# Optimization experiments

Measured on AMD Instinct MI355X. Metric: run time of the kernel, lower is better.

## Reference

```python
import jax, jax.numpy as jnp
import numpy as np

F = 20  # hard-coded feature width in the module


def setup_inputs() -> dict:
    key = jax.random.key(0)
    k1, k2, k3, k4 = jax.random.split(key, 4)
    N = 1048576
    x = jax.random.normal(k1, (N, F), dtype=jnp.float32)
    # nn.Linear(20, 20): weight [out, in], bias [out]
    W = jax.random.normal(k2, (F, F), dtype=jnp.float32) * (1.0 / np.sqrt(F))
    b = jax.random.normal(k3, (F,), dtype=jnp.float32) * 0.01
    rand_weight = jax.random.normal(k4, (F, F), dtype=jnp.float32)
    return {"x": x, "W": W, "b": b, "rand_weight": rand_weight}


def _halving_count(s):
    """Smallest int k >= 0 with s * 2^-k <= 1 (== number of `x /= 2` loop iters)."""
    k = jnp.ceil(jnp.log2(jnp.maximum(s, 1.0))).astype(jnp.int32)
    # guard against float rounding in log2
    k = jnp.where(s * jnp.exp2(-k.astype(jnp.float32)) > 1.0, k + 1, k)
    k = jnp.where((k > 0) & (s * jnp.exp2(-(k - 1).astype(jnp.float32)) <= 1.0), k - 1, k)
    return k


def reference(x, W, b, rand_weight):
    # x = self.linear(x)
    h = x @ W.T + b
    # x = relu(x @ rand_weight + 1)
    h = jax.nn.relu(h @ rand_weight + 1.0)
    # x = self.linear(x)  (shared weights)
    h = h @ W.T + b
    # while x.abs().sum() > 1: x /= 2   ->  x * 2^-k
    s = jnp.sum(jnp.abs(h))
    k = _halving_count(s)
    h = h * jnp.exp2(-k.astype(h.dtype))
    return jnp.sum(h)
```

## Files before the change

kernel.cpp:

```cpp
#include <hip/hip_runtime.h>
#include <math.h>

#define FF 20
#define TPB 256
#define TPW 8

typedef __fp16 half2v __attribute__((ext_vector_type(2)));
typedef __fp16 half8 __attribute__((ext_vector_type(8)));
typedef float f32x4 __attribute__((ext_vector_type(4)));

__global__ void mlp_setup(const float* __restrict__ W, const float* __restrict__ b,
                          const float* __restrict__ R, __fp16* __restrict__ frag) {
    int t = threadIdx.x;
    int f = t >> 6, l = t & 63;
    int g = l >> 4, p = l & 15;
    int row = (f & 1) * 16 + p;
    #pragma unroll
    for (int e = 0; e < 8; ++e) {
        int k = (e < 4) ? (4 * g + e) : (16 + 4 * g + (e - 4));
        float v = 0.f;
        if (f < 2) {
            if (row < FF) {
                if (k < FF) {
                    float s = 0.f;
                    for (int j = 0; j < FF; ++j) s = fmaf(W[j * FF + k], R[j * FF + row], s);
                    v = s;
                } else if (k == FF) {
                    float s = 1.0f;
                    for (int j = 0; j < FF; ++j) s = fmaf(b[j], R[j * FF + row], s);
                    v = s;
                }
            }
        } else {
            if (row < FF) {
                if (k < FF) v = W[row * FF + k];
                else if (k == FF) v = b[row];
            }
        }
        frag[t * 8 + e] = (__fp16)v;
    }
}

__global__ __launch_bounds__(TPB) void mlp_main(
    const float* __restrict__ x, const __fp16* __restrict__ frag,
    double2* __restrict__ partials, int nrows, int ntiles)
{
    const int t = threadIdx.x;
    const int l = t & 63;
    const int g = l >> 4;
    const int r = l & 15;

    const half8 A10 = *reinterpret_cast<const half8*>(frag + (0 * 64 + l) * 8);
    const half8 A11 = *reinterpret_cast<const half8*>(frag + (1 * 64 + l) * 8);
    const half8 A20 = *reinterpret_cast<const half8*>(frag + (2 * 64 + l) * 8);
    const half8 A21 = *reinterpret_cast<const half8*>(frag + (3 * 64 + l) * 8);

    const int wave_id = blockIdx.x * (TPB / 64) + (t >> 6);
    const int base_row = wave_id * (TPW * 16) + r;

    float4 xa[TPW], xb[TPW];
    const float* rowp = x + (size_t)base_row * FF;
    #pragma unroll
    for (int u = 0; u < TPW; ++u) {
        int row = base_row + u * 16;
        xa[u] = make_float4(0.f, 0.f, 0.f, 0.f);
        if (row < nrows)
            xa[u] = *reinterpret_cast<const float4*>(rowp + (size_t)u * 16 * FF + 4 * g);
    }
    #pragma unroll
    for (int u = 0; u < TPW; ++u) {
        int row = base_row + u * 16;
        xb[u] = make_float4(0.f, 0.f, 0.f, 0.f);
        if (g == 0 && row < nrows)
            xb[u] = *reinterpret_cast<const float4*>(rowp + (size_t)u * 16 * FF + 16);
    }

    float psum = 0.f, pabs = 0.f;
    const f32x4 zero = {0.f, 0.f, 0.f, 0.f};

    #pragma unroll
    for (int u = 0; u < TPW; ++u) {
        half8 B1;
        half2v p0 = __builtin_amdgcn_cvt_pkrtz(xa[u].x, xa[u].y);
        half2v p1 = __builtin_amdgcn_cvt_pkrtz(xa[u].z, xa[u].w);
        B1[0] = p0[0]; B1[1] = p0[1]; B1[2] = p1[0]; B1[3] = p1[1];
        if (g == 0) {
            half2v p2 = __builtin_amdgcn_cvt_pkrtz(xb[u].x, xb[u].y);
            half2v p3 = __builtin_amdgcn_cvt_pkrtz(xb[u].z, xb[u].w);
            B1[4] = p2[0]; B1[5] = p2[1]; B1[6] = p3[0]; B1[7] = p3[1];
        } else if (g == 1) {
            B1[4] = (__fp16)1.0f;
            B1[5] = (__fp16)0.f; B1[6] = (__fp16)0.f; B1[7] = (__fp16)0.f;
        } else {
            B1[4] = (__fp16)0.f; B1[5] = (__fp16)0.f;
            B1[6] = (__fp16)0.f; B1[7] = (__fp16)0.f;
        }
        f32x4 c0 = __builtin_amdgcn_mfma_f32_16x16x32_f16(A10, B1, zero, 0, 0, 0);
        f32x4 c1 = __builtin_amdgcn_mfma_f32_16x16x32_f16(A11, B1, zero, 0, 0, 0);
        half8 B2;
        half2v q0 = __builtin_amdgcn_cvt_pkrtz(fmaxf(c0[0], 0.f), fmaxf(c0[1], 0.f));
        half2v q1 = __builtin_amdgcn_cvt_pkrtz(fmaxf(c0[2], 0.f), fmaxf(c0[3], 0.f));
        half2v q2 = __builtin_amdgcn_cvt_pkrtz(fmaxf(c1[0], 0.f), fmaxf(c1[1], 0.f));
        half2v q3 = __builtin_amdgcn_cvt_pkrtz(fmaxf(c1[2], 0.f), fmaxf(c1[3], 0.f));
        B2[0] = q0[0]; B2[1] = q0[1]; B2[2] = q1[0]; B2[3] = q1[1];
        B2[4] = q2[0]; B2[5] = q2[1]; B2[6] = q3[0]; B2[7] = q3[1];
        if (g == 1) B2[4] = (__fp16)1.0f;
        f32x4 d0 = __builtin_amdgcn_mfma_f32_16x16x32_f16(A20, B2, zero, 0, 0, 0);
        f32x4 d1 = __builtin_amdgcn_mfma_f32_16x16x32_f16(A21, B2, zero, 0, 0, 0);
        if (base_row + u * 16 < nrows) {
            #pragma unroll
            for (int q = 0; q < 4; ++q) {
                psum += d0[q];            pabs += fabsf(d0[q]);
                psum += d1[q];            pabs += fabsf(d1[q]);
            }
        }
    }

    #pragma unroll
    for (int off = 32; off > 0; off >>= 1) {
        psum += __shfl_down(psum, off, 64);
        pabs += __shfl_down(pabs, off, 64);
    }
    __shared__ double wsum[TPB / 64], wabs[TPB / 64];
    if ((t & 63) == 0) { wsum[t >> 6] = (double)psum; wabs[t >> 6] = (double)pabs; }
    __syncthreads();
    if (t == 0) {
        double bs = 0.0, ba = 0.0;
        #pragma unroll
        for (int w = 0; w < TPB / 64; ++w) { bs += wsum[w]; ba += wabs[w]; }
        partials[blockIdx.x] = make_double2(bs, ba);
    }
}

__global__ __launch_bounds__(256) void mlp_final(const double2* __restrict__ parts,
                                                 int nparts, float* __restrict__ out) {
    __shared__ double s_sum[256], s_abs[256];
    int t = threadIdx.x;
    double a = 0.0, sg = 0.0;
    for (int i = t; i < nparts; i += 256) { sg += parts[i].x; a += parts[i].y; }
    s_sum[t] = sg; s_abs[t] = a;
    __syncthreads();
    for (int off = 128; off > 0; off >>= 1) {
        if (t < off) { s_sum[t] += s_sum[t + off]; s_abs[t] += s_abs[t + off]; }
        __syncthreads();
    }
    if (t == 0) {
        double s = s_abs[0];
        int k = 0;
        while (s > 1.0 && k < 4000) { s *= 0.5; ++k; }
        out[0] = (float)ldexp(s_sum[0], -k);
    }
}

extern "C" void kernel_launch(void* const* d_in, const int* in_sizes, int n_in,
                              void* d_out, int out_size, void* d_ws, size_t ws_size,
                              hipStream_t stream) {
    const float* x = (const float*)d_in[0];
    const float* W = (const float*)d_in[1];
    const float* b = (const float*)d_in[2];
    const float* R = (const float*)d_in[3];
    float* out = (float*)d_out;

    __fp16* frag = (__fp16*)d_ws;
    double2* partials = (double2*)((char*)d_ws + 8192);

    int nrows = in_sizes[0] / FF;
    int ntiles = (nrows + 15) / 16;
    int waves = (ntiles + TPW - 1) / TPW;
    int blocks = (waves + (TPB / 64) - 1) / (TPB / 64);

    hipLaunchKernelGGL(mlp_setup, dim3(1), dim3(256), 0, stream, W, b, R, frag);
    hipLaunchKernelGGL(mlp_main, dim3(blocks), dim3(TPB), 0, stream,
                       x, frag, partials, nrows, ntiles);
    hipLaunchKernelGGL(mlp_final, dim3(1), dim3(256), 0, stream, partials, blocks, out);
}
```

Baseline: 30.76 us.

## Fuse weight-fragment setup into main kernel via per-wave MFMA precompute

Removes the separate single-block setup kernel and instead has every wave build its MFMA A-fragments directly from W, b and R, computing W^T·R (plus the bias row) with four small MFMAs in registers. This drops one kernel launch and its serialization ahead of the main kernel, at the cost of redundant scattered global loads of the weights and extra MFMAs in every wave. It also splits the load and compute path into a full-tile branch with no per-row bounds checks and a guarded tail branch. Precision changes slightly because the fused matrix is now formed from fp16-rounded inputs instead of being computed in fp32.

```diff
diff --git a/kernel.cpp b/kernel.cpp
--- a/kernel.cpp
+++ b/kernel.cpp
@@ -9,111 +9,130 @@
 typedef __fp16 half8 __attribute__((ext_vector_type(8)));
 typedef float f32x4 __attribute__((ext_vector_type(4)));
 
-__global__ void mlp_setup(const float* __restrict__ W, const float* __restrict__ b,
-                          const float* __restrict__ R, __fp16* __restrict__ frag) {
-    int t = threadIdx.x;
-    int f = t >> 6, l = t & 63;
-    int g = l >> 4, p = l & 15;
-    int row = (f & 1) * 16 + p;
-    #pragma unroll
-    for (int e = 0; e < 8; ++e) {
-        int k = (e < 4) ? (4 * g + e) : (16 + 4 * g + (e - 4));
-        float v = 0.f;
-        if (f < 2) {
-            if (row < FF) {
-                if (k < FF) {
-                    float s = 0.f;
-                    for (int j = 0; j < FF; ++j) s = fmaf(W[j * FF + k], R[j * FF + row], s);
-                    v = s;
-                } else if (k == FF) {
-                    float s = 1.0f;
-                    for (int j = 0; j < FF; ++j) s = fmaf(b[j], R[j * FF + row], s);
-                    v = s;
-                }
-            }
-        } else {
-            if (row < FF) {
-                if (k < FF) v = W[row * FF + k];
-                else if (k == FF) v = b[row];
-            }
-        }
-        frag[t * 8 + e] = (__fp16)v;
+#define MFMA16(A, B, C) __builtin_amdgcn_mfma_f32_16x16x32_f16(A, B, C, 0, 0, 0)
+
+#define TILE_BODY(XA, XB, LIVE)                                                \
+    {                                                                          \
+        half8 B1;                                                              \
+        half2v p0 = __builtin_amdgcn_cvt_pkrtz((XA).x, (XA).y);                \
+        half2v p1 = __builtin_amdgcn_cvt_pkrtz((XA).z, (XA).w);                \
+        B1[0] = p0[0]; B1[1] = p0[1]; B1[2] = p1[0]; B1[3] = p1[1];            \
+        if (g == 0) {                                                          \
+            half2v p2 = __builtin_amdgcn_cvt_pkrtz((XB).x, (XB).y);            \
+            half2v p3 = __builtin_amdgcn_cvt_pkrtz((XB).z, (XB).w);            \
+            B1[4] = p2[0]; B1[5] = p2[1]; B1[6] = p3[0]; B1[7] = p3[1];        \
+        } else if (g == 1) {                                                   \
+            B1[4] = (__fp16)1.0f;         \
+            B1[5] = (__fp16)0.f; B1[6] = (__fp16)0.f; B1[7] = (__fp16)0.f;     \
+        } else {                                                               \
+            B1[4] = (__fp16)0.f; B1[5] = (__fp16)0.f;                          \
+            B1[6] = (__fp16)0.f; B1[7] = (__fp16)0.f;                          \
+        }                                                                      \
+        f32x4 c0 = MFMA16(A10, B1, zero);                                      \
+        f32x4 c1 = MFMA16(A11, B1, zero);                                      \
+        half8 B2;                                                              \
+        half2v q0 = __builtin_amdgcn_cvt_pkrtz(fmaxf(c0[0],0.f), fmaxf(c0[1],0.f)); \
+        half2v q1 = __builtin_amdgcn_cvt_pkrtz(fmaxf(c0[2],0.f), fmaxf(c0[3],0.f)); \
+        half2v q2 = __builtin_amdgcn_cvt_pkrtz(fmaxf(c1[0],0.f), fmaxf(c1[1],0.f)); \
+        half2v q3 = __builtin_amdgcn_cvt_pkrtz(fmaxf(c1[2],0.f), fmaxf(c1[3],0.f)); \
+        B2[0] = q0[0]; B2[1] = q0[1]; B2[2] = q1[0]; B2[3] = q1[1];            \
+        B2[4] = q2[0]; B2[5] = q2[1]; B2[6] = q3[0]; B2[7] = q3[1];            \
+        if (g == 1) B2[4] = (__fp16)1.0f;        \
+        f32x4 d0 = MFMA16(A20, B2, zero);                                      \
+        f32x4 d1 = MFMA16(A21, B2, zero);                                      \
+        if (LIVE) {                                                            \
+            _Pragma("unroll")                                                  \
+            for (int q = 0; q < 4; ++q) {                                      \
+                psum += d0[q]; pabs += fabsf(d0[q]);                           \
+                psum += d1[q]; pabs += fabsf(d1[q]);                           \
+            }                                                                  \
+        }                                                                      \
     }
-}
 
 __global__ __launch_bounds__(TPB) void mlp_main(
-    const float* __restrict__ x, const __fp16* __restrict__ frag,
-    double2* __restrict__ partials, int nrows, int ntiles)
+    const float* __restrict__ x, const float* __restrict__ W,
+    const float* __restrict__ bv, const float* __restrict__ R,
+    double2* __restrict__ partials, int nrows)
 {
     const int t = threadIdx.x;
     const int l = t & 63;
     const int g = l >> 4;
     const int r = l & 15;
 
-    const half8 A10 = *reinterpret_cast<const half8*>(frag + (0 * 64 + l) * 8);
-    const half8 A11 = *reinterpret_cast<const half8*>(frag + (1 * 64 + l) * 8);
-    const half8 A20 = *reinterpret_cast<const half8*>(frag + (2 * 64 + l) * 8);
-    const half8 A21 = *reinterpret_cast<const half8*>(frag + (3 * 64 + l) * 8);
+    half8 AW0, AP, BR0, BR1, A20, A21;
+    #pragma unroll
+    for (int e = 0; e < 8; ++e) {
+        const int j = (e < 4) ? (4 * g + e) : (16 + 4 * g + (e - 4));
+        const bool jv = (j < FF);
+        float aw0 = jv ? W[j * FF + r] : 0.f;
+        float ap = 0.f;
+        if (jv) {
+            if (r < 4)       ap = W[j * FF + 16 + r];
+            else if (r == 4) ap = bv[j];
+        }
+        float br0 = jv ? R[j * FF + r] : 0.f;
+        float br1 = (jv && r < 4) ? R[j * FF + 16 + r] : 0.f;
+        float a20 = jv ? W[r * FF + j] : ((j == FF) ? bv[r] : 0.f);
+        float a21 = 0.f;
+        if (r < 4) a21 = jv ? W[(16 + r) * FF + j] : ((j == FF) ? bv[16 + r] : 0.f);
+        AW0[e] = (__fp16)aw0; AP[e]  = (__fp16)ap;
+        BR0[e] = (__fp16)br0; BR1[e] = (__fp16)br1;
+        A20[e] = (__fp16)a20; A21[e] = (__fp16)a21;
+    }
+    const f32x4 zero = {0.f, 0.f, 0.f, 0.f};
+    f32x4 D00 = MFMA16(AW0, BR0, zero);
+    f32x4 D10 = MFMA16(AP,  BR0, zero);
+    f32x4 D01 = MFMA16(AW0, BR1, zero);
+    f32x4 D11 = MFMA16(AP,  BR1, zero);
+    half8 A10, A11;
+    A10[0] = (__fp16)D00[0]; A10[1] = (__fp16)D00[1];
+    A10[2] = (__fp16)D00[2]; A10[3] = (__fp16)D00[3];
+    A11[0] = (__fp16)D01[0]; A11[1] = (__fp16)D01[1];
+    A11[2] = (__fp16)D01[2]; A11[3] = (__fp16)D01[3];
+    {
+        float v0 = D10[0], v1 = D11[0];
+        if (g == 1) { v0 += 1.f; if (r < 4) v1 += 1.f; }
+        A10[4] = (__fp16)v0;      A11[4] = (__fp16)v1;
+        A10[5] = (__fp16)D10[1];  A11[5] = (__fp16)D11[1];
+        A10[6] = (__fp16)D10[2];  A11[6] = (__fp16)D11[2];
+        A10[7] = (__fp16)D10[3];  A11[7] = (__fp16)D11[3];
+    }
 
     const int wave_id = blockIdx.x * (TPB / 64) + (t >> 6);
-    const int base_row = wave_id * (TPW * 16) + r;
+    const long base_row = (long)wave_id * (TPW * 16) + r;
+    const float* rowp = x + base_row * FF;
+    float psum = 0.f, pabs = 0.f;
+    float4 xa[TPW], xb[TPW];
+    const bool full = ((long)(wave_id + 1) * (TPW * 16)) <= (long)nrows;
 
-    float4 xa[TPW], xb[TPW];
-    const float* rowp = x + (size_t)base_row * FF;
-    #pragma unroll
-    for (int u = 0; u < TPW; ++u) {
-        int row = base_row + u * 16;
-        xa[u] = make_float4(0.f, 0.f, 0.f, 0.f);
-        if (row < nrows)
+    if (full) {
+        #pragma unroll
+        for (int u = 0; u < TPW; ++u)
             xa[u] = *reinterpret_cast<const float4*>(rowp + (size_t)u * 16 * FF + 4 * g);
-    }
-    #pragma unroll
-    for (int u = 0; u < TPW; ++u) {
-        int row = base_row + u * 16;
-        xb[u] = make_float4(0.f, 0.f, 0.f, 0.f);
-        if (g == 0 && row < nrows)
-            xb[u] = *reinterpret_cast<const float4*>(rowp + (size_t)u * 16 * FF + 16);
-    }
-
-    float psum = 0.f, pabs = 0.f;
-    const f32x4 zero = {0.f, 0.f, 0.f, 0.f};
-
-    #pragma unroll
-    for (int u = 0; u < TPW; ++u) {
-        half8 B1;
-        half2v p0 = __builtin_amdgcn_cvt_pkrtz(xa[u].x, xa[u].y);
-        half2v p1 = __builtin_amdgcn_cvt_pkrtz(xa[u].z, xa[u].w);
-        B1[0] = p0[0]; B1[1] = p0[1]; B1[2] = p1[0]; B1[3] = p1[1];
-        if (g == 0) {
-            half2v p2 = __builtin_amdgcn_cvt_pkrtz(xb[u].x, xb[u].y);
-            half2v p3 = __builtin_amdgcn_cvt_pkrtz(xb[u].z, xb[u].w);
-            B1[4] = p2[0]; B1[5] = p2[1]; B1[6] = p3[0]; B1[7] = p3[1];
-        } else if (g == 1) {
-            B1[4] = (__fp16)1.0f;
-            B1[5] = (__fp16)0.f; B1[6] = (__fp16)0.f; B1[7] = (__fp16)0.f;
-        } else {
-            B1[4] = (__fp16)0.f; B1[5] = (__fp16)0.f;
-            B1[6] = (__fp16)0.f; B1[7] = (__fp16)0.f;
+        #pragma unroll
+        for (int u = 0; u < TPW; ++u) {
+            xb[u] = make_float4(0.f, 0.f, 0.f, 0.f);
+            if (g == 0)
+                xb[u] = *reinterpret_cast<const float4*>(rowp + (size_t)u * 16 * FF + 16);
         }
-        f32x4 c0 = __builtin_amdgcn_mfma_f32_16x16x32_f16(A10, B1, zero, 0, 0, 0);
-        f32x4 c1 = __builtin_amdgcn_mfma_f32_16x16x32_f16(A11, B1, zero, 0, 0, 0);
-        half8 B2;
-        half2v q0 = __builtin_amdgcn_cvt_pkrtz(fmaxf(c0[0], 0.f), fmaxf(c0[1], 0.f));
-        half2v q1 = __builtin_amdgcn_cvt_pkrtz(fmaxf(c0[2], 0.f), fmaxf(c0[3], 0.f));
-        half2v q2 = __builtin_amdgcn_cvt_pkrtz(fmaxf(c1[0], 0.f), fmaxf(c1[1], 0.f));
-        half2v q3 = __builtin_amdgcn_cvt_pkrtz(fmaxf(c1[2], 0.f), fmaxf(c1[3], 0.f));
-        B2[0] = q0[0]; B2[1] = q0[1]; B2[2] = q1[0]; B2[3] = q1[1];
-        B2[4] = q2[0]; B2[5] = q2[1]; B2[6] = q3[0]; B2[7] = q3[1];
-        if (g == 1) B2[4] = (__fp16)1.0f;
-        f32x4 d0 = __builtin_amdgcn_mfma_f32_16x16x32_f16(A20, B2, zero, 0, 0, 0);
-        f32x4 d1 = __builtin_amdgcn_mfma_f32_16x16x32_f16(A21, B2, zero, 0, 0, 0);
-        if (base_row + u * 16 < nrows) {
-            #pragma unroll
-            for (int q = 0; q < 4; ++q) {
-                psum += d0[q];            pabs += fabsf(d0[q]);
-                psum += d1[q];            pabs += fabsf(d1[q]);
+        #pragma unroll
+        for (int u = 0; u < TPW; ++u)
+            TILE_BODY(xa[u], xb[u], true);
+    } else {
+        #pragma unroll
+        for (int u = 0; u < TPW; ++u) {
+            long row = base_row + u * 16;
+            xa[u] = make_float4(0.f, 0.f, 0.f, 0.f);
+            xb[u] = make_float4(0.f, 0.f, 0.f, 0.f);
+            if (row < nrows) {
+                xa[u] = *reinterpret_cast<const float4*>(rowp + (size_t)u * 16 * FF + 4 * g);
+                if (g == 0)
+                    xb[u] = *reinterpret_cast<const float4*>(rowp + (size_t)u * 16 * FF + 16);
             }
         }
+        #pragma unroll
+        for (int u = 0; u < TPW; ++u)
+            TILE_BODY(xa[u], xb[u], (base_row + u * 16 < nrows));
     }
 
     #pragma unroll
@@ -157,20 +176,18 @@
                               hipStream_t stream) {
     const float* x = (const float*)d_in[0];
     const float* W = (const float*)d_in[1];
-    const float* b = (const float*)d_in[2];
+    const float* bv = (const float*)d_in[2];
     const float* R = (const float*)d_in[3];
     float* out = (float*)d_out;
 
-    __fp16* frag = (__fp16*)d_ws;
-    double2* partials = (double2*)((char*)d_ws + 8192);
+    double2* partials = (double2*)d_ws;
 
     int nrows = in_sizes[0] / FF;
     int ntiles = (nrows + 15) / 16;
     int waves = (ntiles + TPW - 1) / TPW;
     int blocks = (waves + (TPB / 64) - 1) / (TPB / 64);
 
-    hipLaunchKernelGGL(mlp_setup, dim3(1), dim3(256), 0, stream, W, b, R, frag);
     hipLaunchKernelGGL(mlp_main, dim3(blocks), dim3(TPB), 0, stream,
-                       x, frag, partials, nrows, ntiles);
+                       x, W, bv, R, partials, nrows);
     hipLaunchKernelGGL(mlp_final, dim3(1), dim3(256), 0, stream, partials, blocks, out);
 }
```

Result: slower. 36.51 us (+18.7%).
